# Kernel tuning notes

Measured on AMD Instinct MI355X. Metric: run time of the kernel, lower is better.

The kernel has to match this reference:

```python
import jax, jax.numpy as jnp
import numpy as np

N_NODES = 50000
N_EDGES = 200000
N_GRAPHS = 2048
EMB = 300
N_LAYERS = 5
BN_EPS = 1e-5


def setup_inputs() -> dict:
    key = jax.random.key(0)
    ks = jax.random.split(key, 16)
    s = 0.02
    d = {}
    d["atomic_number"] = jax.random.randint(ks[0], (N_NODES,), 0, 120)
    d["chirality_type"] = jax.random.randint(ks[1], (N_NODES,), 0, 3)
    d["bond_type"] = jax.random.randint(ks[2], (N_EDGES,), 0, 6)
    d["bond_direction_type"] = jax.random.randint(ks[3], (N_EDGES,), 0, 3)
    d["src"] = jax.random.randint(ks[4], (N_EDGES,), 0, N_NODES)
    d["dst"] = jax.random.randint(ks[5], (N_EDGES,), 0, N_NODES)
    d["graph_ids"] = jnp.sort(jax.random.randint(ks[6], (N_NODES,), 0, N_GRAPHS))
    d["num_graphs"] = N_GRAPHS
    d["node_emb0"] = jax.random.normal(ks[7], (120, EMB), jnp.float32) * s
    d["node_emb1"] = jax.random.normal(ks[8], (3, EMB), jnp.float32) * s
    d["edge_emb0"] = jax.random.normal(ks[9], (N_LAYERS, 6, EMB), jnp.float32) * s
    d["edge_emb1"] = jax.random.normal(ks[10], (N_LAYERS, 3, EMB), jnp.float32) * s
    d["W1"] = jax.random.normal(ks[11], (N_LAYERS, EMB, 2 * EMB), jnp.float32) * s
    d["b1"] = jnp.zeros((N_LAYERS, 2 * EMB), jnp.float32)
    d["W2"] = jax.random.normal(ks[12], (N_LAYERS, 2 * EMB, EMB), jnp.float32) * s
    d["b2"] = jnp.zeros((N_LAYERS, EMB), jnp.float32)
    d["bn_gamma"] = jnp.ones((N_LAYERS, EMB), jnp.float32)
    d["bn_beta"] = jnp.zeros((N_LAYERS, EMB), jnp.float32)
    d["bn_mean"] = jax.random.normal(ks[13], (N_LAYERS, EMB), jnp.float32) * s
    d["bn_var"] = jax.random.uniform(ks[14], (N_LAYERS, EMB), jnp.float32, 0.5, 1.5)
    return d


def gin_node_feats(atomic_number, chirality_type, bond_type, bond_direction_type,
                   src, dst, node_emb0, node_emb1, edge_emb0, edge_emb1,
                   W1, b1, W2, b2, bn_gamma, bn_beta, bn_mean, bn_var):
    n = atomic_number.shape[0]
    h = node_emb0[atomic_number] + node_emb1[chirality_type]  # [N, EMB]
    feats = [h]
    for l in range(N_LAYERS):
        # u_add_e message: src node feat + per-layer categorical edge embedding
        e = edge_emb0[l][bond_type] + edge_emb1[l][bond_direction_type]  # [E, EMB]
        m = feats[l][src] + e
        agg = jax.ops.segment_sum(m, dst, num_segments=n)  # sum aggregation at dst
        x = jax.nn.relu(agg @ W1[l] + b1[l]) @ W2[l] + b2[l]  # GIN MLP 300->600->300
        # BatchNorm1d in eval mode (running stats)
        x = (x - bn_mean[l]) * jax.lax.rsqrt(bn_var[l] + BN_EPS) * bn_gamma[l] + bn_beta[l]
        if l < N_LAYERS - 1:
            x = jax.nn.relu(x)  # activation on all but last layer
        feats.append(x)  # dropout is identity in eval mode
    return jnp.concatenate(feats, axis=1)  # JK='concat' -> [N, 6*EMB]


def reference(atomic_number, chirality_type, bond_type, bond_direction_type,
              src, dst, graph_ids, num_graphs,
              node_emb0, node_emb1, edge_emb0, edge_emb1,
              W1, b1, W2, b2, bn_gamma, bn_beta, bn_mean, bn_var):
    nf = gin_node_feats(atomic_number, chirality_type, bond_type, bond_direction_type,
                        src, dst, node_emb0, node_emb1, edge_emb0, edge_emb1,
                        W1, b1, W2, b2, bn_gamma, bn_beta, bn_mean, bn_var)
    sums = jax.ops.segment_sum(nf, graph_ids, num_segments=num_graphs)  # SumPooling
    counts = jax.ops.segment_sum(jnp.ones((nf.shape[0], 1), nf.dtype), graph_ids,
                                 num_segments=num_graphs)
    avg = sums / jnp.maximum(counts, 1.0)  # AvgPooling
    return jnp.concatenate([avg, sums], axis=1)  # [G, 2*6*EMB]
```

## Files before the change

### kernel.cpp

```cpp
#include <hip/hip_runtime.h>

#define EMB 300
#define HID 600
#define NL 5
#define BN_EPS 1e-5f

#define FS 320
#define HS 640
#define NPW 8
#define KS1 10
#define KS2 20

typedef __attribute__((ext_vector_type(8))) short short8;
typedef __attribute__((ext_vector_type(4))) float f32x4;
typedef __attribute__((ext_vector_type(4))) unsigned short us4;

__device__ __forceinline__ unsigned short f2bf(float x) {
    unsigned u = __float_as_uint(x);
    unsigned r = (u + 0x7FFFu + ((u >> 16) & 1u)) >> 16;
    return (unsigned short)r;
}
__device__ __forceinline__ float bf2f(unsigned short h) {
    return __uint_as_float(((unsigned)h) << 16);
}

#define GLDS16(gsrc, ldst)                                                     \
    __builtin_amdgcn_global_load_lds(                                          \
        (const __attribute__((address_space(1))) unsigned int*)(gsrc),         \
        (__attribute__((address_space(3))) unsigned int*)(ldst), 16, 0, 0)

__global__ void k_init_h0(const int* __restrict__ an, const int* __restrict__ ch,
                          const float* __restrict__ ne0, const float* __restrict__ ne1,
                          unsigned short* __restrict__ Fb, int n) {
    int t = blockIdx.x * blockDim.x + threadIdx.x;
    int i = t / (FS / 4), f4 = t - i * (FS / 4);
    if (i >= n) return;
    int f = f4 * 4;
    us4 h = {0, 0, 0, 0};
    if (f < EMB) {
        const float4 a = *(const float4*)(ne0 + (size_t)an[i] * EMB + f);
        const float4 b = *(const float4*)(ne1 + (size_t)ch[i] * EMB + f);
        h[0] = f2bf(a.x + b.x); h[1] = f2bf(a.y + b.y);
        h[2] = f2bf(a.z + b.z); h[3] = f2bf(a.w + b.w);
    }
    *(us4*)(Fb + (size_t)i * FS + f) = h;
}

__global__ void k_hist(const int* __restrict__ dst, const int* __restrict__ bt,
                       const int* __restrict__ bd, int* __restrict__ deg,
                       int* __restrict__ cnt9, int e) {
    int t = blockIdx.x * blockDim.x + threadIdx.x;
    if (t >= e) return;
    int d = dst[t];
    atomicAdd(&deg[d], 1);
    atomicAdd(&cnt9[d * 9 + bt[t]], 1);
    atomicAdd(&cnt9[d * 9 + 6 + bd[t]], 1);
}

__global__ __launch_bounds__(256)
void k_scan_blk(const int* __restrict__ deg, int* __restrict__ incl,
                int* __restrict__ part, int n) {
    int tid = threadIdx.x;
    int base = blockIdx.x * 1024 + tid * 4;
    int v0 = (base + 0 < n) ? deg[base + 0] : 0;
    int v1 = (base + 1 < n) ? deg[base + 1] : 0;
    int v2 = (base + 2 < n) ? deg[base + 2] : 0;
    int v3 = (base + 3 < n) ? deg[base + 3] : 0;
    int ts = v0 + v1 + v2 + v3;
    int lane = tid & 63, w = tid >> 6;
    int x = ts;
#pragma unroll
    for (int off = 1; off < 64; off <<= 1) {
        int y = __shfl_up(x, off);
        if (lane >= off) x += y;
    }
    __shared__ int ws[4];
    if (lane == 63) ws[w] = x;
    __syncthreads();
    int woff = 0;
    for (int i = 0; i < w; ++i) woff += ws[i];
    int r = woff + x - ts;
    r += v0; if (base + 0 < n) incl[base + 0] = r;
    r += v1; if (base + 1 < n) incl[base + 1] = r;
    r += v2; if (base + 2 < n) incl[base + 2] = r;
    r += v3; if (base + 3 < n) incl[base + 3] = r;
    if (tid == 255) part[blockIdx.x] = woff + x;
}

__global__ __launch_bounds__(1024)
void k_scan_part(int* __restrict__ part, int nb) {
    int tid = threadIdx.x;
    int v = (tid < nb) ? part[tid] : 0;
    int lane = tid & 63, w = tid >> 6;
    int x = v;
#pragma unroll
    for (int off = 1; off < 64; off <<= 1) {
        int y = __shfl_up(x, off);
        if (lane >= off) x += y;
    }
    __shared__ int ws[16];
    if (lane == 63) ws[w] = x;
    __syncthreads();
    int woff = 0;
    for (int i = 0; i < w; ++i) woff += ws[i];
    if (tid < nb) part[tid] = woff + x - v;
}

__global__ void k_scan_add(const int* __restrict__ incl, const int* __restrict__ part,
                           const int* __restrict__ deg, int* __restrict__ roff,
                           int* __restrict__ curs, int n) {
    int i = blockIdx.x * blockDim.x + threadIdx.x;
    if (i >= n) return;
    int inc = incl[i] + part[i >> 10];
    roff[i + 1] = inc;
    curs[i] = inc - deg[i];
    if (i == 0) roff[0] = 0;
}

__global__ void k_scatter(const int* __restrict__ dst, const int* __restrict__ src,
                          int* __restrict__ cursor, int* __restrict__ srcs, int e) {
    int t = blockIdx.x * blockDim.x + threadIdx.x;
    if (t < e) { int p = atomicAdd(&cursor[dst[t]], 1); srcs[p] = src[t]; }
}

__global__ void k_gbound(const int* __restrict__ gids, int* __restrict__ gstart,
                         int n, int G) {
    int i = blockIdx.x * blockDim.x + threadIdx.x;
    if (i >= n) return;
    int g = gids[i];
    int gp = (i == 0) ? -1 : gids[i - 1];
    for (int q = gp + 1; q <= g; ++q) gstart[q] = i;
    if (i == n - 1)
        for (int q = g + 1; q <= G; ++q) gstart[q] = n;
}

__global__ void k_prep_w1p(const float* __restrict__ W1, unsigned short* __restrict__ W1P,
                           int total) {
    int t = blockIdx.x * blockDim.x + threadIdx.x;
    if (t >= total) return;
    int lane = t & 63;
    int r = t >> 6;
    int ks = r % KS1; r /= KS1;
    int nf = r % 40;
    int l = r / 40;
    int n = nf * 16 + (lane & 15);
    int kb = ks * 32 + (lane >> 4) * 8;
    unsigned short v[8];
#pragma unroll
    for (int e = 0; e < 8; ++e) {
        int k = kb + e;
        v[e] = (n < HID && k < EMB) ? f2bf(W1[(size_t)l * EMB * HID + (size_t)k * HID + n]) : 0;
    }
    *(short8*)(W1P + (size_t)t * 8) = *(short8*)v;
}

__global__ void k_prep_w2p(const float* __restrict__ W2, unsigned short* __restrict__ W2P,
                           int total) {
    int t = blockIdx.x * blockDim.x + threadIdx.x;
    if (t >= total) return;
    int lane = t & 63;
    int r = t >> 6;
    int ks = r % KS2; r /= KS2;
    int nf = r % 20;
    int l = r / 20;
    int n = nf * 16 + (lane & 15);
    int kb = ks * 32 + (lane >> 4) * 8;
    unsigned short v[8];
#pragma unroll
    for (int e = 0; e < 8; ++e) {
        int k = kb + e;
        v[e] = (n < EMB && k < HID) ? f2bf(W2[(size_t)l * HID * EMB + (size_t)k * EMB + n]) : 0;
    }
    *(short8*)(W2P + (size_t)t * 8) = *(short8*)v;
}

__global__ void k_prep_params(const float* __restrict__ b1, const float* __restrict__ b2,
                              const float* __restrict__ g, const float* __restrict__ be,
                              const float* __restrict__ mu, const float* __restrict__ va,
                              float* __restrict__ b1p, float* __restrict__ scp,
                              float* __restrict__ shp, int total) {
    int t = blockIdx.x * blockDim.x + threadIdx.x;
    if (t >= total) return;
    int n = t % HS, l = t / HS;
    b1p[t] = (n < HID) ? b1[l * HID + n] : 0.f;
    if (n < FS) {
        float sc = 0.f, sh = 0.f;
        if (n < EMB) {
            sc = g[l * EMB + n] * rsqrtf(va[l * EMB + n] + BN_EPS);
            sh = be[l * EMB + n] + (b2[l * EMB + n] - mu[l * EMB + n]) * sc;
        }
        scp[l * FS + n] = sc;
        shp[l * FS + n] = sh;
    }
}

__global__ __launch_bounds__(256)
void k_aggregate(const unsigned short* __restrict__ fb,
                 const float* __restrict__ e0, const float* __restrict__ e1,
                 const int* __restrict__ roff, const int* __restrict__ srcs,
                 const int* __restrict__ cnt9,
                 unsigned short* __restrict__ agg, int n) {
    const int v0 = (blockIdx.x * 4 + (threadIdx.x >> 6)) * NPW;
    if (v0 >= n) return;
    const int lane = threadIdx.x & 63;
    const int nv = min(NPW, n - v0);

    int rv = 0;
    {
        int idx = v0 + lane;
        if (lane <= NPW && idx <= n) rv = roff[idx];
    }
    const int base = __shfl(rv, 0);
    const int total = __shfl(rv, nv) - base;

    const int n9 = n * 9;
    const int base9 = v0 * 9;
    int c0 = (base9 + lane < n9) ? cnt9[base9 + lane] : 0;
    int c1 = (lane < 8 && base9 + 64 + lane < n9) ? cnt9[base9 + 64 + lane] : 0;

    int c = 0;
    int chunk = 0;
    auto nextIdx = [&]() -> int {
        if ((c & 63) == 0)
            chunk = (c + lane < total) ? srcs[base + c + lane] : 0;
        int r = __shfl(chunk, c & 63);
        ++c;
        return r;
    };

#pragma unroll
    for (int i = 0; i < NPW; ++i) {
        if (i < nv) {
            const int di = __shfl(rv, i + 1) - __shfl(rv, i);
            float aA[4] = {0.f, 0.f, 0.f, 0.f};
            float aB[4] = {0.f, 0.f, 0.f, 0.f};
            int k = 0;
            for (; k + 4 <= di; k += 4) {
                int i0 = nextIdx(), i1 = nextIdx(), i2 = nextIdx(), i3 = nextIdx();
                const us4* r0 = (const us4*)(fb + (size_t)i0 * FS);
                const us4* r1 = (const us4*)(fb + (size_t)i1 * FS);
                const us4* r2 = (const us4*)(fb + (size_t)i2 * FS);
                const us4* r3 = (const us4*)(fb + (size_t)i3 * FS);
                us4 x0 = r0[lane], x1 = r1[lane], x2 = r2[lane], x3 = r3[lane];
                us4 y0 = {}, y1 = {}, y2 = {}, y3 = {};
                if (lane < 11) { y0 = r0[64 + lane]; y1 = r1[64 + lane];
                                 y2 = r2[64 + lane]; y3 = r3[64 + lane]; }
#pragma unroll
                for (int q = 0; q < 4; ++q)
                    aA[q] += (bf2f(x0[q]) + bf2f(x1[q])) + (bf2f(x2[q]) + bf2f(x3[q]));
                if (lane < 11) {
#pragma unroll
                    for (int q = 0; q < 4; ++q)
                        aB[q] += (bf2f(y0[q]) + bf2f(y1[q])) + (bf2f(y2[q]) + bf2f(y3[q]));
                }
            }
            for (; k < di; ++k) {
                int i0 = nextIdx();
                const us4* r0 = (const us4*)(fb + (size_t)i0 * FS);
                us4 x0 = r0[lane];
#pragma unroll
                for (int q = 0; q < 4; ++q) aA[q] += bf2f(x0[q]);
                if (lane < 11) {
                    us4 y0 = r0[64 + lane];
#pragma unroll
                    for (int q = 0; q < 4; ++q) aB[q] += bf2f(y0[q]);
                }
            }
#pragma unroll
            for (int t = 0; t < 9; ++t) {
                const int pos = i * 9 + t;
                int cv = __shfl(pos < 64 ? c0 : c1, pos & 63);
                if (cv) {
                    float fc = (float)cv;
                    const float* row = (t < 6) ? (e0 + t * EMB) : (e1 + (t - 6) * EMB);
                    f32x4 ea = *(const f32x4*)(row + 4 * lane);
#pragma unroll
                    for (int q = 0; q < 4; ++q) aA[q] += fc * ea[q];
                    if (lane < 11) {
                        f32x4 eb = *(const f32x4*)(row + 256 + 4 * lane);
#pragma unroll
                        for (int q = 0; q < 4; ++q) aB[q] += fc * eb[q];
                    }
                }
            }
            us4* ar = (us4*)(agg + (size_t)(v0 + i) * FS);
            us4 h;
#pragma unroll
            for (int q = 0; q < 4; ++q) h[q] = f2bf(aA[q]);
            ar[lane] = h;
            if (lane < 11) {
                us4 hb;
#pragma unroll
                for (int q = 0; q < 4; ++q) hb[q] = f2bf(aB[q]);
                ar[64 + lane] = hb;
            }
        }
    }
}

template <int EPI>
__global__ __launch_bounds__(512, 2)
void k_mlp(const unsigned short* __restrict__ A,
           const unsigned short* __restrict__ W1P,
           const unsigned short* __restrict__ W2P,
           const float* __restrict__ b1p,
           const float* __restrict__ scp, const float* __restrict__ shp,
           unsigned short* __restrict__ Cout) {
    __shared__ unsigned short Ash[64 * 320];
    __shared__ unsigned short Hsh[64 * 640];
    const int tid = threadIdx.x;
    const int lane = tid & 63, wid = tid >> 6;
    const int lr = lane & 15, lk = lane >> 4, rgrp = lk * 4;
    const size_t m0s = (size_t)blockIdx.x * 64;

#pragma unroll
    for (int cch = 0; cch < 5; ++cch) {
        const int sbase = wid * 5120 + cch * 1024;
        const int s = sbase + lane * 16;
        const int row = s / 640;
        const int u = s ^ ((row & 7) << 4);
        GLDS16((const char*)A + m0s * 640 + u, (char*)Ash + sbase);
    }
    asm volatile("s_waitcnt vmcnt(0)" ::: "memory");
    __syncthreads();

    {
        f32x4 acc1[5][4] = {};
        short8 bw[5], bn_[5];
#pragma unroll
        for (int i = 0; i < 5; ++i)
            bw[i] = *(const short8*)(W1P + (((size_t)(wid * 5 + i) * KS1 + 0) * 64 + lane) * 8);
        for (int ks = 0; ks < KS1; ++ks) {
            if (ks + 1 < KS1) {
#pragma unroll
                for (int i = 0; i < 5; ++i)
                    bn_[i] = *(const short8*)(W1P + (((size_t)(wid * 5 + i) * KS1 + ks + 1) * 64 + lane) * 8);
            }
            short8 a[4];
#pragma unroll
            for (int j = 0; j < 4; ++j) {
                const int row = j * 16 + lr;
                const int o = (row * 640 + ks * 64 + lk * 16) ^ ((lr & 7) << 4);
                a[j] = *(const short8*)((const char*)Ash + o);
            }
            __builtin_amdgcn_s_setprio(1);
#pragma unroll
            for (int i = 0; i < 5; ++i)
#pragma unroll
                for (int j = 0; j < 4; ++j)
                    acc1[i][j] = __builtin_amdgcn_mfma_f32_16x16x32_bf16(bw[i], a[j], acc1[i][j], 0, 0, 0);
            __builtin_amdgcn_s_setprio(0);
#pragma unroll
            for (int i = 0; i < 5; ++i) bw[i] = bn_[i];
        }
#pragma unroll
        for (int i = 0; i < 5; ++i) {
            const int n0 = wid * 80 + i * 16 + rgrp;
            const f32x4 q0 = *(const f32x4*)&b1p[n0];
#pragma unroll
            for (int j = 0; j < 4; ++j) {
                const int m = j * 16 + lr;
                us4 h;
#pragma unroll
                for (int p = 0; p < 4; ++p)
                    h[p] = f2bf(fmaxf(acc1[i][j][p] + q0[p], 0.f));
                const int o = (m * 1280 + n0 * 2) ^ ((lr & 7) << 4);
                *(us4*)((char*)Hsh + o) = h;
            }
        }
    }
    __syncthreads();

    {
        const int wm2 = wid >> 2, wn2 = wid & 3;
        f32x4 acc2[5][2] = {};
        short8 cw[5], cn_[5];
#pragma unroll
        for (int i = 0; i < 5; ++i)
            cw[i] = *(const short8*)(W2P + (((size_t)(wn2 * 5 + i) * KS2 + 0) * 64 + lane) * 8);
        for (int ks = 0; ks < KS2; ++ks) {
            if (ks + 1 < KS2) {
#pragma unroll
                for (int i = 0; i < 5; ++i)
                    cn_[i] = *(const short8*)(W2P + (((size_t)(wn2 * 5 + i) * KS2 + ks + 1) * 64 + lane) * 8);
            }
            short8 a[2];
#pragma unroll
            for (int j = 0; j < 2; ++j) {
                const int row = wm2 * 32 + j * 16 + lr;
                const int o = (row * 1280 + ks * 64 + lk * 16) ^ ((lr & 7) << 4);
                a[j] = *(const short8*)((const char*)Hsh + o);
            }
            __builtin_amdgcn_s_setprio(1);
#pragma unroll
            for (int i = 0; i < 5; ++i)
#pragma unroll
                for (int j = 0; j < 2; ++j)
                    acc2[i][j] = __builtin_amdgcn_mfma_f32_16x16x32_bf16(cw[i], a[j], acc2[i][j], 0, 0, 0);
            __builtin_amdgcn_s_setprio(0);
#pragma unroll
            for (int i = 0; i < 5; ++i) cw[i] = cn_[i];
        }
#pragma unroll
        for (int i = 0; i < 5; ++i) {
            const int n0 = wn2 * 80 + i * 16 + rgrp;
            const f32x4 q0 = *(const f32x4*)&scp[n0];
            const f32x4 q1 = *(const f32x4*)&shp[n0];
#pragma unroll
            for (int j = 0; j < 2; ++j) {
                const size_t m = m0s + (size_t)(wm2 * 32 + j * 16 + lr);
                us4 h;
#pragma unroll
                for (int p = 0; p < 4; ++p) {
                    float x = acc2[i][j][p] * q0[p] + q1[p];
                    if (EPI == 1) x = fmaxf(x, 0.f);
                    h[p] = f2bf(x);
                }
                *(us4*)(Cout + m * FS + n0) = h;
            }
        }
    }
}

__global__ __launch_bounds__(256)
void k_pool(const unsigned short* __restrict__ feats, const int* __restrict__ gstart,
            float* __restrict__ out, int l) {
    const int g = blockIdx.x;
    const int tid = threadIdx.x;
    const int w = tid >> 6, lane = tid & 63;
    const int s = gstart[g], e = gstart[g + 1];
    float aA[4] = {0.f, 0.f, 0.f, 0.f};
    float aB[4] = {0.f, 0.f, 0.f, 0.f};
    int v = s + w;
    for (; v + 4 < e; v += 8) {
        const us4* r0 = (const us4*)(feats + (size_t)v * FS);
        const us4* r1 = (const us4*)(feats + (size_t)(v + 4) * FS);
        us4 x0 = r0[lane], x1 = r1[lane];
        us4 y0 = {}, y1 = {};
        if (lane < 11) { y0 = r0[64 + lane]; y1 = r1[64 + lane]; }
#pragma unroll
        for (int q = 0; q < 4; ++q) aA[q] += bf2f(x0[q]) + bf2f(x1[q]);
        if (lane < 11) {
#pragma unroll
            for (int q = 0; q < 4; ++q) aB[q] += bf2f(y0[q]) + bf2f(y1[q]);
        }
    }
    if (v < e) {
        const us4* r0 = (const us4*)(feats + (size_t)v * FS);
        us4 x0 = r0[lane];
#pragma unroll
        for (int q = 0; q < 4; ++q) aA[q] += bf2f(x0[q]);
        if (lane < 11) {
            us4 y0 = r0[64 + lane];
#pragma unroll
            for (int q = 0; q < 4; ++q) aB[q] += bf2f(y0[q]);
        }
    }
    __shared__ f32x4 smA[4][64];
    __shared__ f32x4 smB[4][16];
    f32x4 xa;
#pragma unroll
    for (int q = 0; q < 4; ++q) xa[q] = aA[q];
    smA[w][lane] = xa;
    if (lane < 16) {
        f32x4 xb;
#pragma unroll
        for (int q = 0; q < 4; ++q) xb[q] = aB[q];
        smB[w][lane] = xb;
    }
    __syncthreads();
    if (w == 0) {
        f32x4 t = smA[0][lane] + smA[1][lane] + smA[2][lane] + smA[3][lane];
        float inv = 1.0f / fmaxf((float)(e - s), 1.0f);
        float* oavg = out + (size_t)g * (12 * EMB) + l * EMB;
        float* osum = oavg + 6 * EMB;
        *(f32x4*)(oavg + 4 * lane) = t * inv;
        *(f32x4*)(osum + 4 * lane) = t;
        if (lane < 11) {
            f32x4 tb = smB[0][lane] + smB[1][lane] + smB[2][lane] + smB[3][lane];
            *(f32x4*)(oavg + 256 + 4 * lane) = tb * inv;
            *(f32x4*)(osum + 256 + 4 * lane) = tb;
        }
    }
}

extern "C" void kernel_launch(void* const* d_in, const int* in_sizes, int n_in,
                              void* d_out, int out_size, void* d_ws, size_t ws_size,
                              hipStream_t stream) {
    const int*   an  = (const int*)d_in[0];
    const int*   ch  = (const int*)d_in[1];
    const int*   bt  = (const int*)d_in[2];
    const int*   bd  = (const int*)d_in[3];
    const int*   src = (const int*)d_in[4];
    const int*   dst = (const int*)d_in[5];
    const int*   gid = (const int*)d_in[6];
    const float* ne0 = (const float*)d_in[8];
    const float* ne1 = (const float*)d_in[9];
    const float* ee0 = (const float*)d_in[10];
    const float* ee1 = (const float*)d_in[11];
    const float* W1  = (const float*)d_in[12];
    const float* b1  = (const float*)d_in[13];
    const float* W2  = (const float*)d_in[14];
    const float* b2  = (const float*)d_in[15];
    const float* bng = (const float*)d_in[16];
    const float* bnb = (const float*)d_in[17];
    const float* bnm = (const float*)d_in[18];
    const float* bnv = (const float*)d_in[19];

    const int N = in_sizes[0];
    const int E = in_sizes[2];
    const int G = out_size / (12 * EMB);
    const int M_pad = ((N + 63) / 64) * 64;
    const int MT = M_pad / 64;
    const int nb = (N + 1023) / 1024;

    char* ws = (char*)d_ws;
    size_t off = 0;
    auto alloc = [&](size_t bytes) -> void* {
        void* p = (void*)(ws + off);
        off += (bytes + 255) & ~(size_t)255;
        return p;
    };
    unsigned short* Fb0  = (unsigned short*)alloc((size_t)M_pad * FS * 2);
    unsigned short* Fb1  = (unsigned short*)alloc((size_t)M_pad * FS * 2);
    unsigned short* A1   = (unsigned short*)alloc((size_t)M_pad * FS * 2);
    unsigned short* W1P  = (unsigned short*)alloc((size_t)NL * 40 * KS1 * 64 * 8 * 2);
    unsigned short* W2P  = (unsigned short*)alloc((size_t)NL * 20 * KS2 * 64 * 8 * 2);
    float*          b1p  = (float*)alloc((size_t)NL * HS * 4);
    float*          scp  = (float*)alloc((size_t)NL * FS * 4);
    float*          shp  = (float*)alloc((size_t)NL * FS * 4);
    int*            deg  = (int*)alloc((size_t)N * 4);
    int*            roff = (int*)alloc(((size_t)N + 1) * 4);
    int*            curs = (int*)alloc((size_t)N * 4);
    int*            srcs = (int*)alloc((size_t)E * 4);
    int*            cnt9 = (int*)alloc((size_t)N * 9 * 4);
    int*            incl = (int*)alloc((size_t)N * 4);
    int*            part = (int*)alloc((size_t)1024 * 4);
    int*            gst  = (int*)alloc(((size_t)G + 1) * 4);

    {
        int t1 = NL * 40 * KS1 * 64;
        k_prep_w1p<<<(t1 + 255) / 256, 256, 0, stream>>>(W1, W1P, t1);
        int t2 = NL * 20 * KS2 * 64;
        k_prep_w2p<<<(t2 + 255) / 256, 256, 0, stream>>>(W2, W2P, t2);
        int t3 = NL * HS;
        k_prep_params<<<(t3 + 255) / 256, 256, 0, stream>>>(b1, b2, bng, bnb, bnm, bnv,
                                                            b1p, scp, shp, t3);
    }

    {
        int tt = N * (FS / 4);
        k_init_h0<<<(tt + 255) / 256, 256, 0, stream>>>(an, ch, ne0, ne1, Fb0, N);
    }

    hipMemsetAsync(deg, 0, (size_t)N * 4, stream);
    hipMemsetAsync(cnt9, 0, (size_t)N * 9 * 4, stream);
    k_hist<<<(E + 255) / 256, 256, 0, stream>>>(dst, bt, bd, deg, cnt9, E);
    k_scan_blk<<<nb, 256, 0, stream>>>(deg, incl, part, N);
    k_scan_part<<<1, 1024, 0, stream>>>(part, nb);
    k_scan_add<<<(N + 255) / 256, 256, 0, stream>>>(incl, part, deg, roff, curs, N);
    k_scatter<<<(E + 255) / 256, 256, 0, stream>>>(dst, src, curs, srcs, E);
    k_gbound<<<(N + 255) / 256, 256, 0, stream>>>(gid, gst, N, G);

    const int aggBlocks = (N + 4 * NPW - 1) / (4 * NPW);

    unsigned short* Fbc = Fb0;
    unsigned short* Fbo = Fb1;
    for (int l = 0; l < NL; ++l) {
        k_pool<<<G, 256, 0, stream>>>(Fbc, gst, (float*)d_out, l);
        k_aggregate<<<aggBlocks, 256, 0, stream>>>(Fbc,
                                                   ee0 + (size_t)l * 6 * EMB,
                                                   ee1 + (size_t)l * 3 * EMB,
                                                   roff, srcs, cnt9, A1, N);
        const unsigned short* W1Pl = W1P + (size_t)l * 40 * KS1 * 64 * 8;
        const unsigned short* W2Pl = W2P + (size_t)l * 20 * KS2 * 64 * 8;
        if (l < NL - 1)
            k_mlp<1><<<MT, 512, 0, stream>>>(A1, W1Pl, W2Pl,
                                             b1p + (size_t)l * HS,
                                             scp + (size_t)l * FS, shp + (size_t)l * FS,
                                             Fbo);
        else
            k_mlp<2><<<MT, 512, 0, stream>>>(A1, W1Pl, W2Pl,
                                             b1p + (size_t)l * HS,
                                             scp + (size_t)l * FS, shp + (size_t)l * FS,
                                             Fbo);
        unsigned short* t = Fbc; Fbc = Fbo; Fbo = t;
    }
    k_pool<<<G, 256, 0, stream>>>(Fbc, gst, (float*)d_out, NL);
}
```

Measured before the change: 691.7 us.

## Stage MLP weight tiles through double-buffered LDS via async global-to-LDS loads

The fused MLP kernel now streams W1 and W2 fragments into double-buffered LDS regions (reusing the Hsh and Ash buffers while they are idle) using direct global-to-LDS loads, instead of prefetching them into registers. Each k-step issues the next tile's load, reads the current tile from LDS, then waits and barriers. This cuts register pressure and overlaps weight fetch with MFMA work. The cost is an added vmcnt wait and a barrier on every k-step, plus extra LDS traffic.

```diff
diff --git a/kernel.cpp b/kernel.cpp
--- a/kernel.cpp
+++ b/kernel.cpp
@@ -312,6 +312,7 @@
     const int lane = tid & 63, wid = tid >> 6;
     const int lr = lane & 15, lk = lane >> 4, rgrp = lk * 4;
     const size_t m0s = (size_t)blockIdx.x * 64;
+    const int swz = (lr & 7) << 4;
 
 #pragma unroll
     for (int cch = 0; cch < 5; ++cch) {
@@ -321,26 +322,33 @@
         const int u = s ^ ((row & 7) << 4);
         GLDS16((const char*)A + m0s * 640 + u, (char*)Ash + sbase);
     }
+#pragma unroll
+    for (int i = 0; i < 5; ++i) {
+        const int nf = wid * 5 + i;
+        GLDS16(W1P + (((size_t)nf * KS1 + 0) * 64 + lane) * 8, &Hsh[nf * 512]);
+    }
     asm volatile("s_waitcnt vmcnt(0)" ::: "memory");
-    __syncthreads();
-
+    __builtin_amdgcn_s_barrier();
+
+    f32x4 acc1[5][4] = {};
     {
-        f32x4 acc1[5][4] = {};
-        short8 bw[5], bn_[5];
-#pragma unroll
-        for (int i = 0; i < 5; ++i)
-            bw[i] = *(const short8*)(W1P + (((size_t)(wid * 5 + i) * KS1 + 0) * 64 + lane) * 8);
+        int buf = 0;
         for (int ks = 0; ks < KS1; ++ks) {
             if (ks + 1 < KS1) {
 #pragma unroll
-                for (int i = 0; i < 5; ++i)
-                    bn_[i] = *(const short8*)(W1P + (((size_t)(wid * 5 + i) * KS1 + ks + 1) * 64 + lane) * 8);
-            }
-            short8 a[4];
+                for (int i = 0; i < 5; ++i) {
+                    const int nf = wid * 5 + i;
+                    GLDS16(W1P + (((size_t)nf * KS1 + ks + 1) * 64 + lane) * 8,
+                           &Hsh[(buf ^ 1) * 20480 + nf * 512]);
+                }
+            }
+            short8 w[5], a[4];
+#pragma unroll
+            for (int i = 0; i < 5; ++i)
+                w[i] = *(const short8*)&Hsh[buf * 20480 + (wid * 5 + i) * 512 + lane * 8];
 #pragma unroll
             for (int j = 0; j < 4; ++j) {
-                const int row = j * 16 + lr;
-                const int o = (row * 640 + ks * 64 + lk * 16) ^ ((lr & 7) << 4);
+                const int o = ((j * 16 + lr) * 640 + ks * 64 + lk * 16) ^ swz;
                 a[j] = *(const short8*)((const char*)Ash + o);
             }
             __builtin_amdgcn_s_setprio(1);
@@ -348,58 +356,64 @@
             for (int i = 0; i < 5; ++i)
 #pragma unroll
                 for (int j = 0; j < 4; ++j)
-                    acc1[i][j] = __builtin_amdgcn_mfma_f32_16x16x32_bf16(bw[i], a[j], acc1[i][j], 0, 0, 0);
+                    acc1[i][j] = __builtin_amdgcn_mfma_f32_16x16x32_bf16(w[i], a[j], acc1[i][j], 0, 0, 0);
             __builtin_amdgcn_s_setprio(0);
-#pragma unroll
-            for (int i = 0; i < 5; ++i) bw[i] = bn_[i];
-        }
-#pragma unroll
-        for (int i = 0; i < 5; ++i) {
-            const int n0 = wid * 80 + i * 16 + rgrp;
-            const f32x4 q0 = *(const f32x4*)&b1p[n0];
-#pragma unroll
-            for (int j = 0; j < 4; ++j) {
-                const int m = j * 16 + lr;
-                us4 h;
-#pragma unroll
-                for (int p = 0; p < 4; ++p)
-                    h[p] = f2bf(fmaxf(acc1[i][j][p] + q0[p], 0.f));
-                const int o = (m * 1280 + n0 * 2) ^ ((lr & 7) << 4);
-                *(us4*)((char*)Hsh + o) = h;
-            }
-        }
-    }
-    __syncthreads();
+            asm volatile("s_waitcnt vmcnt(0)" ::: "memory");
+            __builtin_amdgcn_s_barrier();
+            buf ^= 1;
+        }
+    }
+
+    for (int c = wid; c < 20; c += 8)
+        GLDS16(W2P + (((size_t)c * KS2 + 0) * 64 + lane) * 8, &Ash[c * 512]);
+
+#pragma unroll
+    for (int i = 0; i < 5; ++i) {
+        const int n0 = wid * 80 + i * 16 + rgrp;
+        const f32x4 q0 = *(const f32x4*)&b1p[n0];
+#pragma unroll
+        for (int j = 0; j < 4; ++j) {
+            const int m = j * 16 + lr;
+            us4 hh;
+#pragma unroll
+            for (int p = 0; p < 4; ++p)
+                hh[p] = f2bf(fmaxf(acc1[i][j][p] + q0[p], 0.f));
+            const int o = (m * 1280 + n0 * 2) ^ swz;
+            *(us4*)((char*)Hsh + o) = hh;
+        }
+    }
+    asm volatile("s_waitcnt vmcnt(0)" ::: "memory");
+    __builtin_amdgcn_s_barrier();
 
     {
         const int wm2 = wid >> 2, wn2 = wid & 3;
+        const int r0 = wm2 * 32 + lr;
         f32x4 acc2[5][2] = {};
-        short8 cw[5], cn_[5];
-#pragma unroll
-        for (int i = 0; i < 5; ++i)
-            cw[i] = *(const short8*)(W2P + (((size_t)(wn2 * 5 + i) * KS2 + 0) * 64 + lane) * 8);
+        int buf = 0;
         for (int ks = 0; ks < KS2; ++ks) {
             if (ks + 1 < KS2) {
-#pragma unroll
-                for (int i = 0; i < 5; ++i)
-                    cn_[i] = *(const short8*)(W2P + (((size_t)(wn2 * 5 + i) * KS2 + ks + 1) * 64 + lane) * 8);
-            }
-            short8 a[2];
-#pragma unroll
-            for (int j = 0; j < 2; ++j) {
-                const int row = wm2 * 32 + j * 16 + lr;
-                const int o = (row * 1280 + ks * 64 + lk * 16) ^ ((lr & 7) << 4);
-                a[j] = *(const short8*)((const char*)Hsh + o);
-            }
+                for (int c = wid; c < 20; c += 8)
+                    GLDS16(W2P + (((size_t)c * KS2 + ks + 1) * 64 + lane) * 8,
+                           &Ash[(buf ^ 1) * 10240 + c * 512]);
+            }
+            short8 w[5];
+#pragma unroll
+            for (int i = 0; i < 5; ++i)
+                w[i] = *(const short8*)&Ash[buf * 10240 + (wn2 * 5 + i) * 512 + lane * 8];
+            const int oh0 = (r0 * 1280 + ks * 64 + lk * 16) ^ swz;
+            const int oh1 = ((r0 + 16) * 1280 + ks * 64 + lk * 16) ^ swz;
+            short8 h0 = *(const short8*)((const char*)Hsh + oh0);
+            short8 h1 = *(const short8*)((const char*)Hsh + oh1);
             __builtin_amdgcn_s_setprio(1);
 #pragma unroll
-            for (int i = 0; i < 5; ++i)
-#pragma unroll
-                for (int j = 0; j < 2; ++j)
-                    acc2[i][j] = __builtin_amdgcn_mfma_f32_16x16x32_bf16(cw[i], a[j], acc2[i][j], 0, 0, 0);
+            for (int i = 0; i < 5; ++i) {
+                acc2[i][0] = __builtin_amdgcn_mfma_f32_16x16x32_bf16(w[i], h0, acc2[i][0], 0, 0, 0);
+                acc2[i][1] = __builtin_amdgcn_mfma_f32_16x16x32_bf16(w[i], h1, acc2[i][1], 0, 0, 0);
+            }
             __builtin_amdgcn_s_setprio(0);
-#pragma unroll
-            for (int i = 0; i < 5; ++i) cw[i] = cn_[i];
+            asm volatile("s_waitcnt vmcnt(0)" ::: "memory");
+            __builtin_amdgcn_s_barrier();
+            buf ^= 1;
         }
 #pragma unroll
         for (int i = 0; i < 5; ++i) {
@@ -409,14 +423,14 @@
 #pragma unroll
             for (int j = 0; j < 2; ++j) {
                 const size_t m = m0s + (size_t)(wm2 * 32 + j * 16 + lr);
-                us4 h;
+                us4 hh;
 #pragma unroll
                 for (int p = 0; p < 4; ++p) {
                     float x = acc2[i][j][p] * q0[p] + q1[p];
                     if (EPI == 1) x = fmaxf(x, 0.f);
-                    h[p] = f2bf(x);
+                    hh[p] = f2bf(x);
                 }
-                *(us4*)(Cout + m * FS + n0) = h;
+                *(us4*)(Cout + m * FS + n0) = hh;
             }
         }
     }
```

Result: slower. 900.0 us (+30.1%).
